# Kernel optimization log

Hardware: AMD Instinct MI355X
Metric: run time of the kernel (lower is better)

Reference implementation:

```python
import jax, jax.numpy as jnp
from jax import lax
import numpy as np

EPS = 1e-7          # BCE clamp
SMOOTH = 1.0        # Dice smoothing
INT_INF = jnp.int32(2**31 - 1)


def _bce_dice(p, t):
    """BCE + Dice loss (standard BCEDiceLoss): p, t float32 in [0,1]."""
    pc = jnp.clip(p, EPS, 1.0 - EPS)
    bce = -jnp.mean(t * jnp.log(pc) + (1.0 - t) * jnp.log1p(-pc))
    inter = jnp.sum(p * t)
    dice = 1.0 - (2.0 * inter + SMOOTH) / (jnp.sum(p) + jnp.sum(t) + SMOOTH)
    return bce + dice


def _ccl(mask):
    """4-connected component labeling per batch image.
    mask: [B,H,W] bool. Returns (labels, init_labels) int32; 0 = background.
    Iterative min-label propagation to a fixpoint (lax.while_loop)."""
    B, H, W = mask.shape
    init = jnp.where(mask, jnp.arange(1, B * H * W + 1, dtype=jnp.int32).reshape(B, H, W), 0)

    def step(lab):
        big = jnp.where(mask, lab, INT_INF)
        pad_h = jnp.full((B, 1, W), INT_INF, jnp.int32)
        pad_w = jnp.full((B, H, 1), INT_INF, jnp.int32)
        up    = jnp.concatenate([big[:, 1:, :], pad_h], axis=1)
        down  = jnp.concatenate([pad_h, big[:, :-1, :]], axis=1)
        left  = jnp.concatenate([big[:, :, 1:], pad_w], axis=2)
        right = jnp.concatenate([pad_w, big[:, :, :-1]], axis=2)
        m = jnp.minimum(big, jnp.minimum(jnp.minimum(up, down), jnp.minimum(left, right)))
        return jnp.where(mask, m, 0)

    def cond(c):
        return c[1]

    def body(c):
        new = step(c[0])
        return (new, jnp.any(new != c[0]))

    lab, _ = lax.while_loop(cond, body, (init, jnp.array(True)))
    return lab, init


def _forward(pred_out, target_mask, num_target_classes):
    f32 = jnp.float32
    B, C, H, W = pred_out.shape
    pred_masks = jnp.argmax(pred_out, axis=1)      # [B,H,W] int
    tm = target_mask[:, 0]                         # [B,H,W] int

    # background-vs-background BCEDice term
    res = _bce_dice((pred_masks == 0).astype(f32), (tm == 0).astype(f32))

    ph = jnp.zeros((B, H, W), f32)    # pred_placeholder
    pho = jnp.zeros((B, H, W), f32)   # pred_placeholder_out
    last_i = jnp.int32(1)

    # fixed loop over predicted classes (torch loops over unique values;
    # here: loop 1..C-1 gated by presence so absent classes are no-ops)
    for v in range(1, C):
        cur = pred_masks == v                       # class-v mask
        present = jnp.any(cur)
        lab, init = _ccl(cur)
        # number of connected components = pixels that kept their seed label
        n_comp = jnp.sum((lab == init) & cur).astype(jnp.int32)
        has_bg = jnp.any(~cur).astype(jnp.int32)    # 0 in cur_uniq?
        # sum_c (c_mask + last_i) over components == cur + n_comp*last_i everywhere
        inc = cur.astype(f32) + (n_comp * last_i).astype(f32)
        ph = jnp.where(present, ph + inc, ph)
        pho = jnp.where(cur, pred_out[:, v], pho)
        last_i = last_i + jnp.where(present, n_comp + has_bg, 0)

    # loop over nonzero target ids (bounded by num_target_classes), gated by presence
    for t in range(1, num_target_classes):
        target_m = tm == t
        present = jnp.any(target_m)
        n = jnp.sum(target_m)
        # torch.median(ph[target_m]): lower median of masked values
        vals = jnp.where(target_m.reshape(-1), ph.reshape(-1), jnp.inf)
        med = jnp.sort(vals)[jnp.maximum((n - 1) // 2, 0)]
        tm_f = target_m.astype(f32)
        contrib = _bce_dice(pho * (ph == med).astype(f32), tm_f)
        extra = jnp.sum(pho * ((ph != med) & target_m).astype(f32)) / jnp.maximum(n, 1).astype(f32)
        res = res + jnp.where(present, contrib + extra, 0.0)

    # len(torch.unique(target_mask)) with values in [0, num_target_classes)
    n_unique = jnp.sum(jnp.stack([jnp.any(tm == t) for t in range(num_target_classes)]).astype(jnp.int32))
    return res / (2 * n_unique + 1).astype(f32)


def setup_inputs() -> dict:
    key = jax.random.key(0)
    k1, k2 = jax.random.split(key)
    B, C, H, W = 8, 5, 768, 768
    pred_out = jax.random.uniform(k1, (B, C, H, W), dtype=jnp.float32)
    target_mask = jax.random.randint(k2, (B, 1, H, W), 0, 4, dtype=jnp.int32)
    return {"pred_out": pred_out, "target_mask": target_mask, "num_target_classes": 4}


def reference(pred_out, target_mask, num_target_classes):
    return _forward(pred_out, target_mask, num_target_classes)
```

## Files before the change

### kernel.cpp

```cpp
#include <hip/hip_runtime.h>
#include <stdint.h>
#include <math.h>

#define B_ 8
#define C_ 5
#define H_ 768
#define W_ 768
#define HW_ (H_*W_)
#define HWq (HW_/4)
#define NPIX (B_*HW_)
#define NQUAD (NPIX/4)
#define TB 8
#define INVAL 0xFFFFFFFFu
#define LN2F 0.69314718056f
#define BIASF 16.2f
#define TILE 64
#define TPR 12
#define TPC 12
#define NTILES (B_*TPR*TPC)
#define NNODES (NTILES*256)
#define SEAMS_PER_IMG (11*768)
#define NB_HALF (B_*SEAMS_PER_IMG)
#define NB_TOT (2*NB_HALF)
#define SEAMBLK (NB_TOT/256)
#define SBLK 2304
#define NTH (SBLK*256)

typedef unsigned long long ull;

static __device__ __forceinline__ unsigned pload(const unsigned* P, unsigned i) {
  return __hip_atomic_load(&P[i], __ATOMIC_RELAXED, __HIP_MEMORY_SCOPE_AGENT);
}
static __device__ unsigned findRootG(unsigned* P, unsigned i) {
  unsigned p = pload(P, i);
  if (p == i) return i;
  unsigned gp = pload(P, p);
  while (p != gp) {
    __hip_atomic_store(&P[i], gp, __ATOMIC_RELAXED, __HIP_MEMORY_SCOPE_AGENT);
    i = p; p = gp; gp = pload(P, p);
  }
  return p;
}
static __device__ bool uniteG(unsigned* P, unsigned a, unsigned b) {
  a = findRootG(P, a);
  b = findRootG(P, b);
  while (a != b) {
    if (a < b) { unsigned t = a; a = b; b = t; }
    unsigned old = atomicCAS(&P[a], a, b);
    if (old == a) return true;
    a = findRootG(P, old);
    b = findRootG(P, b);
  }
  return false;
}
static __device__ __forceinline__ unsigned ploadL(const unsigned* P, unsigned i) {
  return __hip_atomic_load(&P[i], __ATOMIC_RELAXED, __HIP_MEMORY_SCOPE_WORKGROUP);
}
static __device__ unsigned findRootL(const unsigned* P, unsigned i) {
  unsigned p = ploadL(P, i) & 0xFFFFu;
  while (p != i) { i = p; p = ploadL(P, i) & 0xFFFFu; }
  return i;
}
static __device__ void uniteL(unsigned* P, unsigned a, unsigned b) {
  a = findRootL(P, a);
  b = findRootL(P, b);
  while (a != b) {
    if (a < b) { unsigned t = a; a = b; b = t; }
    unsigned old = atomicCAS(&P[a], 0xFFFF0000u | a, 0xFFFF0000u | b);
    if (old == (0xFFFF0000u | a)) return;
    a = findRootL(P, old & 0xFFFFu);
    b = findRootL(P, b);
  }
}

__global__ __launch_bounds__(256) void k_stats(
    const float4* __restrict__ pred4, const int4* __restrict__ tgt4,
    unsigned* __restrict__ cls4, double* __restrict__ sp)
{
  __shared__ ull h[32][41];
  for (int i = threadIdx.x; i < 32*41; i += 256) (&h[0][0])[i] = 0ull;
  __syncthreads();
  const int cp = threadIdx.x & 31;
  const int tid = blockIdx.x * 256 + threadIdx.x;

#define DOQUAD(P0, P1, P2, P3, P4, T4, PACKED)                                 \
  {                                                                            \
    PACKED = 0u;                                                               \
    _Pragma("unroll")                                                          \
    for (int j = 0; j < 4; ++j) {                                              \
      float v0 = ((const float*)&(P0))[j];                                     \
      float v1 = ((const float*)&(P1))[j];                                     \
      float v2 = ((const float*)&(P2))[j];                                     \
      float v3 = ((const float*)&(P3))[j];                                     \
      float v4 = ((const float*)&(P4))[j];                                     \
      int tt = ((const int*)&(T4))[j];                                         \
      float best = v0; int bc = 0;                                             \
      if (v1 > best) { best = v1; bc = 1; }                                    \
      if (v2 > best) { best = v2; bc = 2; }                                    \
      if (v3 > best) { best = v3; bc = 3; }                                    \
      if (v4 > best) { best = v4; bc = 4; }                                    \
      unsigned tu = (unsigned)tt; if (tu >= TB) tu = TB - 1;                   \
      ull w;                                                                   \
      if (bc) {                                                                \
        float pc = fminf(fmaxf(best, 1e-7f), 1.0f - 1e-7f);                    \
        float l2p = __log2f(pc);                                               \
        float l2m = __log2f(1.0f - pc);                                        \
        float logit = (l2p - l2m) * LN2F;                                      \
        float mag   = -l2m * LN2F;                                             \
        w = (1ull << 57)                                                       \
          | ((ull)__float2uint_rn(best * 4096.0f) << 38)                       \
          | ((ull)__float2uint_rn((logit + BIASF) * 64.0f) << 20)              \
          | (ull)__float2uint_rn(mag * 64.0f);                                 \
      } else {                                                                 \
        w = 1ull << 57;                                                        \
      }                                                                        \
      atomicAdd(&h[cp][(int)tu * C_ + bc], w);                                 \
      PACKED |= ((unsigned)bc) << (8 * j);                                     \
    }                                                                          \
  }

  {
    int q0 = tid;
    int q1 = tid + NTH;
    int b0 = q0 / HWq, h0 = q0 - b0 * HWq;
    int b1 = q1 / HWq, h1 = q1 - b1 * HWq;
    const float4* ba = pred4 + (size_t)b0 * (C_*HWq) + h0;
    const float4* bb = pred4 + (size_t)b1 * (C_*HWq) + h1;
    float4 a0 = ba[0], a1 = ba[HWq], a2 = ba[2*HWq], a3 = ba[3*HWq], a4 = ba[4*HWq];
    float4 c0 = bb[0], c1 = bb[HWq], c2 = bb[2*HWq], c3 = bb[3*HWq], c4 = bb[4*HWq];
    int4 ta = tgt4[q0];
    int4 tb = tgt4[q1];
    unsigned pk0, pk1;
    DOQUAD(a0, a1, a2, a3, a4, ta, pk0)
    DOQUAD(c0, c1, c2, c3, c4, tb, pk1)
    cls4[q0] = pk0;
    cls4[q1] = pk1;
  }
#undef DOQUAD
  __syncthreads();
  if (threadIdx.x < 160) {
    int slot = threadIdx.x >> 2, comp = threadIdx.x & 3;
    double s = 0.0;
#pragma unroll
    for (int c = 0; c < 32; ++c) {
      ull w = h[c][slot];
      if (comp == 0)      s += (double)(w >> 57);
      else if (comp == 1) s += (double)((w >> 38) & 0x7FFFFull) * (1.0/4096.0);
      else if (comp == 2) s += (double)((w >> 20) & 0x3FFFFull) * (1.0/64.0);
      else                s += (double)(w & 0x1FFFFull) * (1.0/64.0);
    }
    sp[(size_t)blockIdx.x * 160 + threadIdx.x] = s;
  }
}

__global__ __launch_bounds__(256) void k_ccl(
    const unsigned* __restrict__ cls4, unsigned short* __restrict__ border,
    unsigned* __restrict__ P2, unsigned* __restrict__ rootcnt)
{
  __shared__ unsigned lab[TILE*TILE];
  __shared__ unsigned lclsw[TILE*TILE/4];
  __shared__ unsigned s_rt[4];
  unsigned char* lcls = (unsigned char*)lclsw;

  int blk = blockIdx.x;
  int b = blk / (TPR*TPC);
  int rem = blk - b * (TPR*TPC);
  int ty0 = (rem / TPR) * TILE;
  int tx0 = (rem - (rem / TPR) * TPR) * TILE;

  if (threadIdx.x < 4) s_rt[threadIdx.x] = 0u;
  {
    unsigned n = (unsigned)blk * 256u + threadIdx.x;
    P2[n] = n;
  }
  const int r = threadIdx.x >> 2, cq = threadIdx.x & 3;
  const int seg = r * 64 + cq * 16;
  union { uint4 q; unsigned char bch[16]; unsigned w[4]; } A, D;
  {
    const uint4* src = (const uint4*)(cls4 + ((b * HW_ + (ty0 + r) * W_ + tx0) >> 2));
    A.q = src[cq];
    *(uint4*)&lclsw[r * 16 + cq * 4] = A.q;
  }
#pragma unroll
  for (int m = 0; m < 4; ++m) {
    uint4 lw;
    unsigned* lp = (unsigned*)&lw;
#pragma unroll
    for (int k = 0; k < 4; ++k) {
      int li = seg + m * 4 + k;
      unsigned c = (A.w[m] >> (8 * k)) & 255u;
      lp[k] = c ? (0xFFFF0000u | (unsigned)li) : INVAL;
    }
    *(uint4*)&lab[seg + m * 4] = lw;
  }
  __syncthreads();

  bool hasDown = (r < 63);
  if (hasDown) D.q = *(const uint4*)&lclsw[(r + 1) * 16 + cq * 4];
  else D.q = make_uint4(0, 0, 0, 0);
  unsigned rb = (cq < 3) ? (unsigned)lcls[seg + 16] : 0u;
#pragma unroll
  for (int j = 0; j < 16; ++j) {
    unsigned c = A.bch[j];
    if (!c) continue;
    int li = seg + j;
    unsigned cr = (j < 15) ? (unsigned)A.bch[j + 1] : rb;
    if (cr == c) uniteL(lab, li, li + 1);
    if (D.bch[j] == c) uniteL(lab, li, li + 64);
  }
  __syncthreads();

#pragma unroll
  for (int m = 0; m < 4; ++m) {
    uint4 lw = *(const uint4*)&lab[seg + m * 4];
    const unsigned* lp = (const unsigned*)&lw;
#pragma unroll
    for (int k = 0; k < 4; ++k) {
      int li = seg + m * 4 + k;
      unsigned c = A.bch[m * 4 + k];
      if (c && (lp[k] & 0xFFFFu) == (unsigned)li) atomicAdd(&s_rt[c - 1], 1u);
    }
  }
  int bp = threadIdx.x;
  int tx, ty;
  if (bp < 64)       { ty = 0;  tx = bp; }
  else if (bp < 128) { ty = 63; tx = bp - 64; }
  else if (bp < 192) { tx = 0;  ty = bp - 128; }
  else               { tx = 63; ty = bp - 192; }
  int li = ty * 64 + tx;
  unsigned char c = lcls[li];
  unsigned rt = 0;
  if (c) {
    rt = findRootL(lab, (unsigned)li);
    atomicMin(&lab[rt], ((unsigned)bp << 16) | rt);
  }
  __syncthreads();
  unsigned sub = c ? (lab[rt] >> 16) : 0u;
  border[blk * 256 + bp] = (unsigned short)(((unsigned)c << 8) | sub);
  if (threadIdx.x < 4) rootcnt[blk * 4 + threadIdx.x] = s_rt[threadIdx.x];
}

__global__ __launch_bounds__(256) void k_seam(const unsigned short* __restrict__ border,
                                              unsigned* __restrict__ P2,
                                              unsigned* __restrict__ smcnt,
                                              const double* __restrict__ sp,
                                              double* __restrict__ spf)
{
  __shared__ unsigned s_sub[4];
  __shared__ double red[256];
  if (threadIdx.x < 4) s_sub[threadIdx.x] = 0u;
  __syncthreads();
  int idx = blockIdx.x * blockDim.x + threadIdx.x;
  if (idx < NB_TOT) {
    int tA, tB, pA, pB;
    if (idx < NB_HALF) {
      int b = idx / SEAMS_PER_IMG;
      int r = idx - b * SEAMS_PER_IMG;
      int seam = r / W_;
      int x = r - seam * W_;
      int tj = x >> 6, k = x & 63;
      tA = (b * TPC + seam) * TPR + tj;
      tB = tA + TPR;
      pA = tA * 256 + 64 + k;
      pB = tB * 256 + 0 + k;
    } else {
      int i2 = idx - NB_HALF;
      int b = i2 / SEAMS_PER_IMG;
      int r = i2 - b * SEAMS_PER_IMG;
      int seam = r / H_;
      int y = r - seam * H_;
      int ti = y >> 6, k = y & 63;
      tA = (b * TPC + ti) * TPR + seam;
      tB = tA + 1;
      pA = tA * 256 + 192 + k;
      pB = tB * 256 + 128 + k;
    }
    unsigned a16 = border[pA];
    unsigned b16 = border[pB];
    unsigned ca = a16 >> 8, cb = b16 >> 8;
    if (ca && ca == cb) {
      if (uniteG(P2, (unsigned)tA * 256u + (a16 & 255u),
                     (unsigned)tB * 256u + (b16 & 255u)))
        atomicAdd(&s_sub[ca - 1], 1u);
    }
  }
  __syncthreads();
  if (threadIdx.x < 4) smcnt[blockIdx.x * 4 + threadIdx.x] = s_sub[threadIdx.x];
  if (blockIdx.x < 160) {
    double s = 0.0;
    for (int j = threadIdx.x; j < SBLK; j += 256) s += sp[(size_t)j * 160 + blockIdx.x];
    red[threadIdx.x] = s;
    __syncthreads();
    for (int off = 128; off; off >>= 1) {
      if (threadIdx.x < off) red[threadIdx.x] += red[threadIdx.x + off];
      __syncthreads();
    }
    if (threadIdx.x == 0) spf[blockIdx.x] = red[0];
  }
}

#define SH_CNT(t,c)   shist[((t)*C_+(c))*4 + 0]
#define SH_PRED(t,c)  shist[((t)*C_+(c))*4 + 1]
#define SH_LRAW(t,c)  shist[((t)*C_+(c))*4 + 2]
#define SH_MAG(t,c)   shist[((t)*C_+(c))*4 + 3]
__global__ __launch_bounds__(256) void k_final(
    const double* __restrict__ spf, const unsigned* __restrict__ rootcnt,
    const unsigned* __restrict__ smcnt, const int* __restrict__ ntcp,
    float* __restrict__ out)
{
  __shared__ double shist[160];
  __shared__ double s_col[C_][3];
  __shared__ unsigned s_cnti[TB*C_];
  __shared__ unsigned s_ctot[C_];
  __shared__ unsigned s_nc[4], s_sm[4];
  __shared__ float s_ph[C_];
  __shared__ double s_term[TB];
  __shared__ int s_NT;
  __shared__ int s_nun;

  if (threadIdx.x < 4) { s_nc[threadIdx.x] = 0u; s_sm[threadIdx.x] = 0u; }
  if (threadIdx.x < TB) s_term[threadIdx.x] = 0.0;
  __syncthreads();
  if (threadIdx.x < 160) shist[threadIdx.x] = spf[threadIdx.x];
  {
    unsigned a = 0;
    for (int j = threadIdx.x; j < NTILES * 4; j += 256) a += rootcnt[j];
    if (a) atomicAdd(&s_nc[threadIdx.x & 3], a);
  }
  {
    unsigned a = 0;
    for (int j = threadIdx.x; j < SEAMBLK * 4; j += 256) a += smcnt[j];
    if (a) atomicAdd(&s_sm[threadIdx.x & 3], a);
  }
  if (threadIdx.x == 0) {
    int NT = ntcp[0];
    if (NT < 1) NT = 1;
    if (NT > TB) NT = TB;
    s_NT = NT;
  }
  __syncthreads();

  if (threadIdx.x < TB * C_) s_cnti[threadIdx.x] = (unsigned)llrint(shist[threadIdx.x * 4]);
  __syncthreads();

  if (threadIdx.x < C_) {
    int c = threadIdx.x;
    double sc = 0.0, sp2 = 0.0, sl = 0.0;
    unsigned ct = 0;
#pragma unroll
    for (int t = 0; t < TB; ++t) {
      sc += SH_CNT(t, c);
      sp2 += SH_PRED(t, c);
      sl += -SH_MAG(t, c);
      ct += s_cnti[t * C_ + c];
    }
    s_col[c][0] = sc; s_col[c][1] = sp2; s_col[c][2] = sl;
    s_ctot[c] = ct;
  }
  __syncthreads();

  if (threadIdx.x == 0) {
#pragma unroll
    for (int cc = 0; cc < C_; ++cc) {
      float ph = 0.0f;
      int li = 1;
#pragma unroll
      for (int v = 1; v < C_; ++v) {
        unsigned ncv = s_nc[v - 1] - s_sm[v - 1];
        if (s_ctot[v] > 0) {
          int prod = (int)(ncv * (unsigned)li);
          float sv = (float)prod;
          float inc = ((cc == v) ? 1.0f : 0.0f) + sv;
          ph = ph + inc;
          li = li + (int)ncv + ((s_ctot[v] < (unsigned)NPIX) ? 1 : 0);
        }
      }
      s_ph[cc] = ph;
    }
  }
  __syncthreads();

  const float EPSF = 1e-7f;
  const double L1 = (double)logf(1.0f - EPSF);
  const double M1 = (double)log1pf(-(1.0f - EPSF));
  const double L0 = (double)logf(EPSF);
  const double M0 = (double)log1pf(-EPSF);
  const double N = (double)NPIX;
  const double BIASD = (double)BIASF;
  const int NT = s_NT;

  if (threadIdx.x == 0) {
    double nt0 = 0;
#pragma unroll
    for (int c = 0; c < C_; ++c) nt0 += SH_CNT(0, c);
    double np1 = (double)s_ctot[0];
    double n11 = SH_CNT(0, 0);
    s_term[0] = -(n11*L1 + (nt0 - n11)*L0 + (np1 - n11)*M1 + (N - nt0 - np1 + n11)*M0) / N
                + 1.0 - (2.0*n11 + 1.0) / (np1 + nt0 + 1.0);
    int nun = 0;
    for (int t = 0; t < NT; ++t) {
      long long s = 0;
#pragma unroll
      for (int c = 0; c < C_; ++c) s += (long long)s_cnti[t * C_ + c];
      if (s) nun++;
    }
    s_nun = nun;
  } else if (threadIdx.x < (unsigned)NT) {
    int t = threadIdx.x;
    long long ntti = 0;
#pragma unroll
    for (int c = 0; c < C_; ++c) ntti += (long long)s_cnti[t * C_ + c];
    if (ntti != 0) {
      double ntt = 0;
#pragma unroll
      for (int c = 0; c < C_; ++c) ntt += SH_CNT(t, c);
      float ph0 = s_ph[0], ph1 = s_ph[1], ph2 = s_ph[2], ph3 = s_ph[3], ph4 = s_ph[4];
      float pht[C_] = {ph0, ph1, ph2, ph3, ph4};
      int idx[C_] = {0, 1, 2, 3, 4};
#pragma unroll
      for (int i = 1; i < C_; ++i)
        for (int j = i; j > 0 && pht[idx[j]] < pht[idx[j-1]]; --j) {
          int tmp = idx[j]; idx[j] = idx[j-1]; idx[j-1] = tmp;
        }
      long long k = (ntti - 1) / 2;
      float med = pht[idx[C_ - 1]];
      long long cum = 0;
#pragma unroll
      for (int i = 0; i < C_; ++i) {
        cum += (long long)s_cnti[t * C_ + idx[i]];
        if (cum > k) { med = pht[idx[i]]; break; }
      }
      double A = 0, Bt = 0, inter = 0, sum_p = 0, ex = 0, nfg_t = 0, nfg_all = 0;
#pragma unroll
      for (int c = 1; c < C_; ++c) {
        double cnt_tc = SH_CNT(t, c);
        double mag_tc = SH_MAG(t, c);
        double spred_tc = SH_PRED(t, c);
        if (pht[c] == med) {
          double logit = SH_LRAW(t, c) - BIASD * cnt_tc;
          A += logit - mag_tc;
          inter += spred_tc;
          nfg_t += cnt_tc;
          nfg_all += s_col[c][0];
          sum_p += s_col[c][1];
          Bt += s_col[c][2] - (-mag_tc);
        } else {
          ex += spred_tc;
        }
      }
      double bce  = -(A + Bt + (ntt - nfg_t)*L0 + (N - ntt - (nfg_all - nfg_t))*M0) / N;
      double dice = 1.0 - (2.0*inter + 1.0) / (sum_p + ntt + 1.0);
      s_term[t] = bce + dice + ex / ntt;
    }
  }
  __syncthreads();
  if (threadIdx.x == 0) {
    double res = 0.0;
#pragma unroll
    for (int t = 0; t < TB; ++t) res += s_term[t];
    out[0] = (float)(res / (double)(2 * s_nun + 1));
  }
}

extern "C" void kernel_launch(void* const* d_in, const int* in_sizes, int n_in,
                              void* d_out, int out_size, void* d_ws, size_t ws_size,
                              hipStream_t stream) {
  const float* pred = (const float*)d_in[0];
  const int* tgt = (const int*)d_in[1];
  const int* ntc = (const int*)d_in[2];
  float* out = (float*)d_out;
  char* ws = (char*)d_ws;
  size_t off = 0;
  unsigned* cls4 = (unsigned*)(ws + off);        off += (size_t)NQUAD * 4;
  double* sp = (double*)(ws + off);              off += (size_t)SBLK * 160 * 8;
  double* spf = (double*)(ws + off);             off += 160 * 8;
  unsigned* P2 = (unsigned*)(ws + off);          off += (size_t)NNODES * 4;
  unsigned short* border = (unsigned short*)(ws + off); off += (size_t)NTILES * 256 * 2;
  unsigned* rootcnt = (unsigned*)(ws + off);     off += (size_t)NTILES * 4 * 4;
  unsigned* smcnt = (unsigned*)(ws + off);       off += (size_t)SEAMBLK * 4 * 4;

  hipLaunchKernelGGL(k_stats, dim3(SBLK), dim3(256), 0, stream,
                     (const float4*)pred, (const int4*)tgt, cls4, sp);
  hipLaunchKernelGGL(k_ccl, dim3(NTILES), dim3(256), 0, stream,
                     cls4, border, P2, rootcnt);
  hipLaunchKernelGGL(k_seam, dim3(SEAMBLK), dim3(256), 0, stream,
                     border, P2, smcnt, sp, spf);
  hipLaunchKernelGGL(k_final, dim3(1), dim3(256), 0, stream,
                     spf, rootcnt, smcnt, ntc, out);
}
```

Before: 200.3 us.

## Fuse argmax/stats kernel into tiled CCL kernel, drop class-map round trip

Merges the per-pixel argmax/histogram kernel into the tile-based CCL kernel, so each 64x64 tile block reads pred and target directly, computes classes and stats, and labels in shared memory. This removes the packed class buffer write and re-read and one kernel launch. In exchange the grid drops from 2304 to 1152 blocks, each processing 16 pixels per thread with more shared memory, which may lower occupancy and latency hiding on the bandwidth-bound read of pred.

Result: slower. 219.4 us (+9.5%).

```diff
diff --git a/kernel.cpp b/kernel.cpp
--- a/kernel.cpp
+++ b/kernel.cpp
@@ -9,7 +9,6 @@
 #define HW_ (H_*W_)
 #define HWq (HW_/4)
 #define NPIX (B_*HW_)
-#define NQUAD (NPIX/4)
 #define TB 8
 #define INVAL 0xFFFFFFFFu
 #define LN2F 0.69314718056f
@@ -23,8 +22,6 @@
 #define NB_HALF (B_*SEAMS_PER_IMG)
 #define NB_TOT (2*NB_HALF)
 #define SEAMBLK (NB_TOT/256)
-#define SBLK 2304
-#define NTH (SBLK*256)
 
 typedef unsigned long long ull;
 
@@ -73,24 +70,42 @@
   }
 }
 
-__global__ __launch_bounds__(256) void k_stats(
-    const float4* __restrict__ pred4, const int4* __restrict__ tgt4,
-    unsigned* __restrict__ cls4, double* __restrict__ sp)
+__global__ __launch_bounds__(256) void k_stats_ccl(
+    const float* __restrict__ pred, const int* __restrict__ tgt,
+    unsigned short* __restrict__ border, unsigned* __restrict__ P2,
+    unsigned* __restrict__ rootcnt, double* __restrict__ sp)
 {
   __shared__ ull h[32][41];
+  __shared__ unsigned lab[TILE*TILE];
+  __shared__ unsigned lclsw[TILE*TILE/4];
+  __shared__ unsigned s_rt[4];
+  unsigned char* lcls = (unsigned char*)lclsw;
+
   for (int i = threadIdx.x; i < 32*41; i += 256) (&h[0][0])[i] = 0ull;
-  __syncthreads();
+  if (threadIdx.x < 4) s_rt[threadIdx.x] = 0u;
+  {
+    unsigned n = (unsigned)blockIdx.x * 256u + threadIdx.x;
+    P2[n] = n;
+  }
+  __syncthreads();
+
   const int cp = threadIdx.x & 31;
-  const int tid = blockIdx.x * 256 + threadIdx.x;
-
-#define DOQUAD(P0, P1, P2, P3, P4, T4, PACKED)                                 \
+  int blk = blockIdx.x;
+  int b = blk / (TPR*TPC);
+  int rem = blk - b * (TPR*TPC);
+  int ty0 = (rem / TPR) * TILE;
+  int tx0 = (rem - (rem / TPR) * TPR) * TILE;
+  const int r = threadIdx.x >> 2, cq = threadIdx.x & 3;
+  const int seg = r * 64 + cq * 16;
+
+#define DOQUAD(P0, P1, P2_, P3, P4, T4, PACKED)                                \
   {                                                                            \
     PACKED = 0u;                                                               \
     _Pragma("unroll")                                                          \
     for (int j = 0; j < 4; ++j) {                                              \
       float v0 = ((const float*)&(P0))[j];                                     \
       float v1 = ((const float*)&(P1))[j];                                     \
-      float v2 = ((const float*)&(P2))[j];                                     \
+      float v2 = ((const float*)&(P2_))[j];                                    \
       float v3 = ((const float*)&(P3))[j];                                     \
       float v4 = ((const float*)&(P4))[j];                                     \
       int tt = ((const int*)&(T4))[j];                                         \
@@ -119,68 +134,26 @@
     }                                                                          \
   }
 
-  {
-    int q0 = tid;
-    int q1 = tid + NTH;
-    int b0 = q0 / HWq, h0 = q0 - b0 * HWq;
-    int b1 = q1 / HWq, h1 = q1 - b1 * HWq;
-    const float4* ba = pred4 + (size_t)b0 * (C_*HWq) + h0;
-    const float4* bb = pred4 + (size_t)b1 * (C_*HWq) + h1;
-    float4 a0 = ba[0], a1 = ba[HWq], a2 = ba[2*HWq], a3 = ba[3*HWq], a4 = ba[4*HWq];
-    float4 c0 = bb[0], c1 = bb[HWq], c2 = bb[2*HWq], c3 = bb[3*HWq], c4 = bb[4*HWq];
-    int4 ta = tgt4[q0];
-    int4 tb = tgt4[q1];
-    unsigned pk0, pk1;
-    DOQUAD(a0, a1, a2, a3, a4, ta, pk0)
-    DOQUAD(c0, c1, c2, c3, c4, tb, pk1)
-    cls4[q0] = pk0;
-    cls4[q1] = pk1;
-  }
-#undef DOQUAD
-  __syncthreads();
-  if (threadIdx.x < 160) {
-    int slot = threadIdx.x >> 2, comp = threadIdx.x & 3;
-    double s = 0.0;
-#pragma unroll
-    for (int c = 0; c < 32; ++c) {
-      ull w = h[c][slot];
-      if (comp == 0)      s += (double)(w >> 57);
-      else if (comp == 1) s += (double)((w >> 38) & 0x7FFFFull) * (1.0/4096.0);
-      else if (comp == 2) s += (double)((w >> 20) & 0x3FFFFull) * (1.0/64.0);
-      else                s += (double)(w & 0x1FFFFull) * (1.0/64.0);
-    }
-    sp[(size_t)blockIdx.x * 160 + threadIdx.x] = s;
-  }
-}
-
-__global__ __launch_bounds__(256) void k_ccl(
-    const unsigned* __restrict__ cls4, unsigned short* __restrict__ border,
-    unsigned* __restrict__ P2, unsigned* __restrict__ rootcnt)
-{
-  __shared__ unsigned lab[TILE*TILE];
-  __shared__ unsigned lclsw[TILE*TILE/4];
-  __shared__ unsigned s_rt[4];
-  unsigned char* lcls = (unsigned char*)lclsw;
-
-  int blk = blockIdx.x;
-  int b = blk / (TPR*TPC);
-  int rem = blk - b * (TPR*TPC);
-  int ty0 = (rem / TPR) * TILE;
-  int tx0 = (rem - (rem / TPR) * TPR) * TILE;
-
-  if (threadIdx.x < 4) s_rt[threadIdx.x] = 0u;
-  {
-    unsigned n = (unsigned)blk * 256u + threadIdx.x;
-    P2[n] = n;
-  }
-  const int r = threadIdx.x >> 2, cq = threadIdx.x & 3;
-  const int seg = r * 64 + cq * 16;
   union { uint4 q; unsigned char bch[16]; unsigned w[4]; } A, D;
   {
-    const uint4* src = (const uint4*)(cls4 + ((b * HW_ + (ty0 + r) * W_ + tx0) >> 2));
-    A.q = src[cq];
-    *(uint4*)&lclsw[r * 16 + cq * 4] = A.q;
-  }
+    const size_t inplane = (size_t)(ty0 + r) * W_ + tx0 + cq * 16;
+    const float4* pp = (const float4*)pred + (((size_t)b * C_ * HW_ + inplane) >> 2);
+    const int4*   tp = (const int4*)tgt   + (((size_t)b * HW_ + inplane) >> 2);
+#pragma unroll
+    for (int m = 0; m < 4; ++m) {
+      float4 a0 = pp[m];
+      float4 a1 = pp[m + HWq];
+      float4 a2 = pp[m + 2*HWq];
+      float4 a3 = pp[m + 3*HWq];
+      float4 a4 = pp[m + 4*HWq];
+      int4 t4 = tp[m];
+      unsigned pk;
+      DOQUAD(a0, a1, a2, a3, a4, t4, pk)
+      A.w[m] = pk;
+    }
+  }
+#undef DOQUAD
+  *(uint4*)&lclsw[r * 16 + cq * 4] = A.q;
 #pragma unroll
   for (int m = 0; m < 4; ++m) {
     uint4 lw;
@@ -238,6 +211,19 @@
   unsigned sub = c ? (lab[rt] >> 16) : 0u;
   border[blk * 256 + bp] = (unsigned short)(((unsigned)c << 8) | sub);
   if (threadIdx.x < 4) rootcnt[blk * 4 + threadIdx.x] = s_rt[threadIdx.x];
+  if (threadIdx.x < 160) {
+    int slot = threadIdx.x >> 2, comp = threadIdx.x & 3;
+    double s = 0.0;
+#pragma unroll
+    for (int cc = 0; cc < 32; ++cc) {
+      ull w = h[cc][slot];
+      if (comp == 0)      s += (double)(w >> 57);
+      else if (comp == 1) s += (double)((w >> 38) & 0x7FFFFull) * (1.0/4096.0);
+      else if (comp == 2) s += (double)((w >> 20) & 0x3FFFFull) * (1.0/64.0);
+      else                s += (double)(w & 0x1FFFFull) * (1.0/64.0);
+    }
+    sp[(size_t)blk * 160 + threadIdx.x] = s;
+  }
 }
 
 __global__ __launch_bounds__(256) void k_seam(const unsigned short* __restrict__ border,
@@ -288,7 +274,7 @@
   if (threadIdx.x < 4) smcnt[blockIdx.x * 4 + threadIdx.x] = s_sub[threadIdx.x];
   if (blockIdx.x < 160) {
     double s = 0.0;
-    for (int j = threadIdx.x; j < SBLK; j += 256) s += sp[(size_t)j * 160 + blockIdx.x];
+    for (int j = threadIdx.x; j < NTILES; j += 256) s += sp[(size_t)j * 160 + blockIdx.x];
     red[threadIdx.x] = s;
     __syncthreads();
     for (int off = 128; off; off >>= 1) {
@@ -471,18 +457,15 @@
   float* out = (float*)d_out;
   char* ws = (char*)d_ws;
   size_t off = 0;
-  unsigned* cls4 = (unsigned*)(ws + off);        off += (size_t)NQUAD * 4;
-  double* sp = (double*)(ws + off);              off += (size_t)SBLK * 160 * 8;
+  double* sp = (double*)(ws + off);              off += (size_t)NTILES * 160 * 8;
   double* spf = (double*)(ws + off);             off += 160 * 8;
   unsigned* P2 = (unsigned*)(ws + off);          off += (size_t)NNODES * 4;
   unsigned short* border = (unsigned short*)(ws + off); off += (size_t)NTILES * 256 * 2;
   unsigned* rootcnt = (unsigned*)(ws + off);     off += (size_t)NTILES * 4 * 4;
   unsigned* smcnt = (unsigned*)(ws + off);       off += (size_t)SEAMBLK * 4 * 4;
 
-  hipLaunchKernelGGL(k_stats, dim3(SBLK), dim3(256), 0, stream,
-                     (const float4*)pred, (const int4*)tgt, cls4, sp);
-  hipLaunchKernelGGL(k_ccl, dim3(NTILES), dim3(256), 0, stream,
-                     cls4, border, P2, rootcnt);
+  hipLaunchKernelGGL(k_stats_ccl, dim3(NTILES), dim3(256), 0, stream,
+                     pred, tgt, border, P2, rootcnt, sp);
   hipLaunchKernelGGL(k_seam, dim3(SEAMBLK), dim3(256), 0, stream,
                      border, P2, smcnt, sp, spf);
   hipLaunchKernelGGL(k_final, dim3(1), dim3(256), 0, stream,
```
